# Performance work log

Hardware: AMD Instinct MI355X
Metric: run time of the kernel (lower is better)

Reference implementation:

```python
import jax, jax.numpy as jnp
import numpy as np
import math

B, L, D = 4, 2048, 1024        # batch, x_len, x_dim
QKV, H = 64, 16                # qkv_dim, head_dim (number of heads)


def setup_inputs() -> dict:
    key = jax.random.key(0)
    ks = jax.random.split(key, 10)
    s = 1.0 / math.sqrt(D)
    return {
        "x": jax.random.normal(ks[0], (B, L, D), jnp.float32),
        "encoder_x": jax.random.normal(ks[1], (B, L, D), jnp.float32),
        "Wq": jax.random.normal(ks[2], (D, QKV * H), jnp.float32) * s,
        "bq": jax.random.normal(ks[3], (QKV * H,), jnp.float32) * 0.01,
        "Wk": jax.random.normal(ks[4], (D, QKV * H), jnp.float32) * s,
        "bk": jax.random.normal(ks[5], (QKV * H,), jnp.float32) * 0.01,
        "Wv": jax.random.normal(ks[6], (D, QKV * H), jnp.float32) * s,
        "bv": jax.random.normal(ks[7], (QKV * H,), jnp.float32) * 0.01,
        "Wo": jax.random.normal(ks[8], (QKV * H, D), jnp.float32) * s,
        "bo": jax.random.normal(ks[9], (D,), jnp.float32) * 0.01,
    }


def reference(x, encoder_x, Wq, bq, Wk, bk, Wv, bv, Wo, bo):
    # q,k from encoder_x; v from x  -> [B, L, H, QKV]
    q = (encoder_x @ Wq + bq).reshape(B, L, H, QKV)
    k = (encoder_x @ Wk + bk).reshape(B, L, H, QKV)
    v = (x @ Wv + bv).reshape(B, L, H, QKV)
    # explicit [B,H,L,L] score matrix + softmax over k (faithful to source)
    scores = jax.nn.softmax(
        jnp.einsum("bqhd,bkhd->bhqk", q, k) / math.sqrt(QKV), axis=-1
    )
    # faithful to source einsum 'bvhd,bhqk->bvhd': no shared contraction
    # index, so scores are summed over (q,k) and broadcast onto v per (b,h).
    attn = jnp.einsum("bvhd,bhqk->bvhd", v, scores).reshape(B, L, H * QKV)
    return attn @ Wo + bo
```

## Files before the change

### kernel.cpp

```cpp
#include <hip/hip_runtime.h>
#include <stdint.h>


typedef __attribute__((ext_vector_type(8))) short bf16x8;
typedef __attribute__((ext_vector_type(4))) float f32x4;

typedef __attribute__((address_space(1))) void as1_void;
typedef __attribute__((address_space(3))) void as3_void;
#define GLD16(g, s)                                                          \
  __builtin_amdgcn_global_load_lds((as1_void*)(g), (as3_void*)(s), 16, 0, 0)

__device__ __forceinline__ short f2bf(float f) {
  union { float f; uint32_t u; } v; v.f = f;
  uint32_t r = v.u + 0x7FFFu + ((v.u >> 16) & 1u);
  return (short)(r >> 16);
}

__device__ __forceinline__ bf16x8 pack8(f32x4 a, f32x4 b) {
  union { f32x4 f; uint32_t u[4]; } x, y;
  x.f = a; y.f = b;
#pragma unroll
  for (int t = 0; t < 4; ++t) x.u[t] += 0x8000u;
#pragma unroll
  for (int t = 0; t < 4; ++t) y.u[t] += 0x8000u;
  union { bf16x8 v; uint32_t u[4]; } o;
  o.u[0] = __builtin_amdgcn_perm(x.u[1], x.u[0], 0x07060302);
  o.u[1] = __builtin_amdgcn_perm(x.u[3], x.u[2], 0x07060302);
  o.u[2] = __builtin_amdgcn_perm(y.u[1], y.u[0], 0x07060302);
  o.u[3] = __builtin_amdgcn_perm(y.u[3], y.u[2], 0x07060302);
  return o.v;
}

__global__ __launch_bounds__(256) void wgemm(
    const float* __restrict__ Wo, const float* __restrict__ Wv,
    const float* __restrict__ bv, const float* __restrict__ bo,
    short* __restrict__ Wt, float* __restrict__ biasc) {
  constexpr int BK = 64, NW = 1024;
  __shared__ __align__(16) float Bsf[64 * BK];
  __shared__ __align__(16) float Ts[64 * 36];
  const int b = blockIdx.x, tid = threadIdx.x;

  if (b >= 512) {
    float* red = Bsf;
    const int b3 = b - 512;
    const int nx = tid & 15, ky = tid >> 4;
    const int n = b3 * 16 + nx;
    float s = 0.f;
    for (int k = ky; k < 1024; k += 16)
      s += bv[k] * Wo[(size_t)k * NW + n];
    red[tid] = s;
    __syncthreads();
#pragma unroll
    for (int st = 128; st >= 16; st >>= 1) {
      if (tid < st) red[tid] += red[tid + st];
      __syncthreads();
    }
    if (ky == 0) biasc[n] = 2048.0f * red[nx] + bo[n];
    return;
  }

  const int lane = tid & 63, wave = tid >> 6;
  const int bm = (b >> 4) * 32, bn = (b & 15) * 64;
  const int wm = (wave & 1) * 16, wn = (wave >> 1) * 32;
  const int l15 = lane & 15, quad = lane >> 4;

  f32x4 acc[2];
  acc[0] = (f32x4){0.f, 0.f, 0.f, 0.f};
  acc[1] = (f32x4){0.f, 0.f, 0.f, 0.f};

  const int br = tid >> 4, bc4 = (tid & 15) ^ (br & 7);
  const float* pb = Wv + (size_t)(bn + br) * NW + bc4 * 4;
  float* lb = Bsf + tid * 4;

  const int ajr = tid >> 3, ac4 = (tid & 7) * 4;
  const float* pa = Wo + (size_t)ajr * NW + bm + ac4;

  for (int kt = 0; kt < 1024; kt += BK) {
    float4 va = *(const float4*)(pa);
    float4 vb = *(const float4*)(pa + 32 * (size_t)NW);
    pa += (size_t)BK * NW;
#pragma unroll
    for (int s = 0; s < 4; ++s) GLD16(pb + (size_t)(16 * s) * NW, lb + 1024 * s);
    pb += BK;
    *(float4*)(Ts + ajr * 36 + ac4) = va;
    *(float4*)(Ts + (ajr + 32) * 36 + ac4) = vb;
    __syncthreads();
#pragma unroll
    for (int kk = 0; kk < 2; ++kk) {
      const float* tsp = Ts + ((kk * 4 + quad) * 8) * 36 + wm + l15;
      float av[8];
#pragma unroll
      for (int e = 0; e < 8; ++e) av[e] = tsp[e * 36];
      bf16x8 af = pack8((f32x4){av[0], av[1], av[2], av[3]},
                        (f32x4){av[4], av[5], av[6], av[7]});
#pragma unroll
      for (int j = 0; j < 2; ++j) {
        const int rn = wn + j * 16 + l15;
        const int c4 = kk * 8 + quad * 2;
        f32x4 u0 = *(const f32x4*)(Bsf + (rn * 16 + (c4 ^ (rn & 7))) * 4);
        f32x4 u1 = *(const f32x4*)(Bsf + (rn * 16 + ((c4 + 1) ^ (rn & 7))) * 4);
        acc[j] = __builtin_amdgcn_mfma_f32_16x16x32_bf16(af, pack8(u0, u1),
                                                         acc[j], 0, 0, 0);
      }
    }
    __syncthreads();
  }
#pragma unroll
  for (int j = 0; j < 2; ++j) {
    const int col = bn + wn + j * 16 + l15;
    const int row0 = bm + wm + quad * 4;
#pragma unroll
    for (int r = 0; r < 4; ++r)
      Wt[(size_t)(row0 + r) * NW + col] = f2bf(2048.f * acc[j][r]);
  }
}

__global__ __launch_bounds__(256) void gemm_main(
    const float* __restrict__ X, const short* __restrict__ Bt,
    const float* __restrict__ bias, float* __restrict__ Out,
    int M, int N, int K) {
  constexpr int BK = 64;
  __shared__ __align__(16) char smem[32768];
  short* As = (short*)smem;
  short* Bs = (short*)(smem + 16384);
  const int tid = threadIdx.x, lane = tid & 63, wave = tid >> 6;
  const int b = blockIdx.x;
  const int bm = (b & 63) * 128;
  const int bn = (b >> 6) * 128;
  const int wm = (wave & 1) * 64, wn = (wave >> 1) * 64;
  const int l15 = lane & 15, quad = lane >> 4;

  f32x4 acc[4][4];
#pragma unroll
  for (int i = 0; i < 4; ++i)
#pragma unroll
    for (int j = 0; j < 4; ++j) acc[i][j] = (f32x4){0.f, 0.f, 0.f, 0.f};

  const int srow = tid >> 3, sc8 = (tid & 7) ^ (srow & 7);
  const float* pa = X + (size_t)(bm + srow) * K + sc8 * 8;
  const short* pb = Bt + (size_t)(bn + srow) * K + sc8 * 8;
  short* la = As + tid * 8;
  short* lb = Bs + tid * 8;

  for (int kt = 0; kt < K; kt += BK) {
    float4 a0[4], a1[4];
#pragma unroll
    for (int s = 0; s < 4; ++s) {
      const float* p = pa + (size_t)(32 * s) * K;
      a0[s] = *(const float4*)(p);
      a1[s] = *(const float4*)(p + 4);
    }
#pragma unroll
    for (int s = 0; s < 4; ++s) GLD16(pb + (size_t)(32 * s) * K, lb + 2048 * s);
    pa += BK; pb += BK;
#pragma unroll
    for (int s = 0; s < 4; ++s) {
      *(bf16x8*)(la + 2048 * s) =
          pack8((f32x4){a0[s].x, a0[s].y, a0[s].z, a0[s].w},
                (f32x4){a1[s].x, a1[s].y, a1[s].z, a1[s].w});
    }
    __syncthreads();
#pragma unroll
    for (int kk = 0; kk < 2; ++kk) {
      bf16x8 af[4], bfr[4];
#pragma unroll
      for (int i = 0; i < 4; ++i) {
        const int r = wm + i * 16 + l15;
        af[i] = *(const bf16x8*)(As + r * BK + ((kk * 4 + quad) ^ (r & 7)) * 8);
      }
#pragma unroll
      for (int j = 0; j < 4; ++j) {
        const int r = wn + j * 16 + l15;
        bfr[j] = *(const bf16x8*)(Bs + r * BK + ((kk * 4 + quad) ^ (r & 7)) * 8);
      }
#pragma unroll
      for (int i = 0; i < 4; ++i)
#pragma unroll
        for (int j = 0; j < 4; ++j)
          acc[i][j] = __builtin_amdgcn_mfma_f32_16x16x32_bf16(
              af[i], bfr[j], acc[i][j], 0, 0, 0);
    }
    __syncthreads();
  }

  float* T = (float*)smem + wave * 1088;
#pragma unroll
  for (int i = 0; i < 4; ++i) {
#pragma unroll
    for (int j = 0; j < 4; ++j) {
      const float bb = bias[bn + wn + j * 16 + l15];
#pragma unroll
      for (int r = 0; r < 4; ++r)
        T[(quad * 4 + r) * 68 + j * 16 + l15] = acc[i][j][r] + bb;
    }
#pragma unroll
    for (int p = 0; p < 4; ++p) {
      const int row = (lane >> 4) + 4 * p;
      const int ch = lane & 15;
      f32x4 v = *(const f32x4*)(T + row * 68 + ch * 4);
      *(f32x4*)(Out + (size_t)(bm + wm + i * 16 + row) * N + bn + wn +
                ch * 4) = v;
    }
  }
}

extern "C" void kernel_launch(void* const* d_in, const int* in_sizes, int n_in,
                              void* d_out, int out_size, void* d_ws,
                              size_t ws_size, hipStream_t stream) {
  const float* x  = (const float*)d_in[0];
  const float* Wv = (const float*)d_in[6];
  const float* bv = (const float*)d_in[7];
  const float* Wo = (const float*)d_in[8];
  const float* bo = (const float*)d_in[9];
  float* out = (float*)d_out;

  constexpr int D = 1024, NO = 1024;
  constexpr int M = 8192;

  char* ws = (char*)d_ws;
  short* wt_bf = (short*)(ws);
  float* biasc = (float*)(ws + (2u << 20));

  wgemm<<<576, 256, 0, stream>>>(Wo, Wv, bv, bo, wt_bf, biasc);
  gemm_main<<<(M / 128) * (NO / 128), 256, 0, stream>>>(
      x, wt_bf, biasc, out, M, NO, D);
}
```

Before: 165.3 us.

## Double-buffer A in LDS, load B fragments to registers, halve N tile

Restructures the main GEMM so A tiles are double-buffered in LDS with software prefetch of the next K slice while the current one computes. B fragments are now read directly from global into registers instead of staged through LDS, and the block tile shrinks from 128x128 to 128x64 to double the grid and raise occupancy (launch bounds 4). The aim is to hide global load latency and increase parallelism. The cost is that A is re-read twice as often and B register loads are uncoalesced per lane.

```diff
diff --git a/kernel.cpp b/kernel.cpp
--- a/kernel.cpp
+++ b/kernel.cpp
@@ -115,91 +115,120 @@
   }
 }
 
-__global__ __launch_bounds__(256) void gemm_main(
+__global__ __launch_bounds__(256, 4) void gemm_main(
     const float* __restrict__ X, const short* __restrict__ Bt,
     const float* __restrict__ bias, float* __restrict__ Out,
     int M, int N, int K) {
   constexpr int BK = 64;
   __shared__ __align__(16) char smem[32768];
-  short* As = (short*)smem;
-  short* Bs = (short*)(smem + 16384);
+  short* As0 = (short*)smem;
+  short* As1 = (short*)(smem + 16384);
   const int tid = threadIdx.x, lane = tid & 63, wave = tid >> 6;
   const int b = blockIdx.x;
   const int bm = (b & 63) * 128;
-  const int bn = (b >> 6) * 128;
-  const int wm = (wave & 1) * 64, wn = (wave >> 1) * 64;
+  const int bn = (b >> 6) * 64;
+  const int wm = (wave & 1) * 64, wn = (wave >> 1) * 32;
   const int l15 = lane & 15, quad = lane >> 4;
 
-  f32x4 acc[4][4];
+  f32x4 acc[4][2];
 #pragma unroll
   for (int i = 0; i < 4; ++i)
 #pragma unroll
-    for (int j = 0; j < 4; ++j) acc[i][j] = (f32x4){0.f, 0.f, 0.f, 0.f};
+    for (int j = 0; j < 2; ++j) acc[i][j] = (f32x4){0.f, 0.f, 0.f, 0.f};
 
   const int srow = tid >> 3, sc8 = (tid & 7) ^ (srow & 7);
   const float* pa = X + (size_t)(bm + srow) * K + sc8 * 8;
-  const short* pb = Bt + (size_t)(bn + srow) * K + sc8 * 8;
-  short* la = As + tid * 8;
-  short* lb = Bs + tid * 8;
-
-  for (int kt = 0; kt < K; kt += BK) {
-    float4 a0[4], a1[4];
-#pragma unroll
-    for (int s = 0; s < 4; ++s) {
-      const float* p = pa + (size_t)(32 * s) * K;
-      a0[s] = *(const float4*)(p);
-      a1[s] = *(const float4*)(p + 4);
-    }
-#pragma unroll
-    for (int s = 0; s < 4; ++s) GLD16(pb + (size_t)(32 * s) * K, lb + 2048 * s);
-    pa += BK; pb += BK;
-#pragma unroll
-    for (int s = 0; s < 4; ++s) {
-      *(bf16x8*)(la + 2048 * s) =
-          pack8((f32x4){a0[s].x, a0[s].y, a0[s].z, a0[s].w},
-                (f32x4){a1[s].x, a1[s].y, a1[s].z, a1[s].w});
-    }
-    __syncthreads();
-#pragma unroll
-    for (int kk = 0; kk < 2; ++kk) {
-      bf16x8 af[4], bfr[4];
-#pragma unroll
-      for (int i = 0; i < 4; ++i) {
-        const int r = wm + i * 16 + l15;
-        af[i] = *(const bf16x8*)(As + r * BK + ((kk * 4 + quad) ^ (r & 7)) * 8);
-      }
-#pragma unroll
-      for (int j = 0; j < 4; ++j) {
-        const int r = wn + j * 16 + l15;
-        bfr[j] = *(const bf16x8*)(Bs + r * BK + ((kk * 4 + quad) ^ (r & 7)) * 8);
-      }
-#pragma unroll
-      for (int i = 0; i < 4; ++i)
-#pragma unroll
-        for (int j = 0; j < 4; ++j)
-          acc[i][j] = __builtin_amdgcn_mfma_f32_16x16x32_bf16(
-              af[i], bfr[j], acc[i][j], 0, 0, 0);
-    }
-    __syncthreads();
-  }
-
-  float* T = (float*)smem + wave * 1088;
+  short* la0 = As0 + tid * 8;
+  short* la1 = As1 + tid * 8;
+
+  const short* pb0 = Bt + (size_t)(bn + wn + l15) * K + quad * 8;
+  const short* pb1 = pb0 + 16 * (size_t)K;
+
+  float4 a0[4], a1[4];
+  bf16x8 Bc[4], Bn[4];
+
+#define LOADA(kt)                                                            \
+  {                                                                          \
+    _Pragma("unroll") for (int s = 0; s < 4; ++s) {                          \
+      const float* p = pa + (size_t)(32 * s) * K + (kt);                     \
+      a0[s] = *(const float4*)(p);                                           \
+      a1[s] = *(const float4*)(p + 4);                                       \
+    }                                                                        \
+  }
+#define LOADB(Br, kt)                                                        \
+  {                                                                          \
+    Br[0] = *(const bf16x8*)(pb0 + (kt));                                    \
+    Br[1] = *(const bf16x8*)(pb1 + (kt));                                    \
+    Br[2] = *(const bf16x8*)(pb0 + (kt) + 32);                               \
+    Br[3] = *(const bf16x8*)(pb1 + (kt) + 32);                               \
+  }
+#define PACKWRITE(la)                                                        \
+  {                                                                          \
+    _Pragma("unroll") for (int s = 0; s < 4; ++s)                            \
+        *(bf16x8*)((la) + 2048 * s) =                                        \
+            pack8((f32x4){a0[s].x, a0[s].y, a0[s].z, a0[s].w},               \
+                  (f32x4){a1[s].x, a1[s].y, a1[s].z, a1[s].w});              \
+  }
+#define COMPUTE(As, Br)                                                      \
+  {                                                                          \
+    _Pragma("unroll") for (int kk = 0; kk < 2; ++kk) {                       \
+      bf16x8 af[4];                                                          \
+      _Pragma("unroll") for (int i = 0; i < 4; ++i) {                        \
+        const int r = wm + i * 16 + l15;                                     \
+        af[i] =                                                              \
+            *(const bf16x8*)((As) + r * BK + ((kk * 4 + quad) ^ (r & 7)) * 8);\
+      }                                                                      \
+      _Pragma("unroll") for (int i = 0; i < 4; ++i)                          \
+          _Pragma("unroll") for (int j = 0; j < 2; ++j)                      \
+              acc[i][j] = __builtin_amdgcn_mfma_f32_16x16x32_bf16(           \
+                  af[i], Br[kk * 2 + j], acc[i][j], 0, 0, 0);                \
+    }                                                                        \
+  }
+
+  LOADA(0);
+  LOADB(Bc, 0);
+  PACKWRITE(la0);
+  __syncthreads();
+
+  for (int trip = 0; trip < 8; ++trip) {
+    const int kt_o = trip * 128 + 64;
+    LOADA(kt_o);
+    LOADB(Bn, kt_o);
+    COMPUTE(As0, Bc);
+    PACKWRITE(la1);
+    __syncthreads();
+    if (trip < 7) {
+      const int kt_n = trip * 128 + 128;
+      LOADA(kt_n);
+      LOADB(Bc, kt_n);
+      COMPUTE(As1, Bn);
+      PACKWRITE(la0);
+    } else {
+      COMPUTE(As1, Bn);
+    }
+    __syncthreads();
+  }
+#undef LOADA
+#undef LOADB
+#undef PACKWRITE
+#undef COMPUTE
+
+  float* T = (float*)smem + wave * 576;
 #pragma unroll
   for (int i = 0; i < 4; ++i) {
 #pragma unroll
-    for (int j = 0; j < 4; ++j) {
+    for (int j = 0; j < 2; ++j) {
       const float bb = bias[bn + wn + j * 16 + l15];
 #pragma unroll
       for (int r = 0; r < 4; ++r)
-        T[(quad * 4 + r) * 68 + j * 16 + l15] = acc[i][j][r] + bb;
-    }
-#pragma unroll
-    for (int p = 0; p < 4; ++p) {
-      const int row = (lane >> 4) + 4 * p;
-      const int ch = lane & 15;
-      f32x4 v = *(const f32x4*)(T + row * 68 + ch * 4);
+        T[(quad * 4 + r) * 36 + j * 16 + l15] = acc[i][j][r] + bb;
+    }
+#pragma unroll
+    for (int c = 0; c < 2; ++c) {
+      const int row = (lane >> 3) + 8 * c;
+      f32x4 v = *(const f32x4*)(T + row * 36 + (lane & 7) * 4);
       *(f32x4*)(Out + (size_t)(bm + wm + i * 16 + row) * N + bn + wn +
-                ch * 4) = v;
+                (lane & 7) * 4) = v;
     }
   }
 }
@@ -222,6 +251,6 @@
   float* biasc = (float*)(ws + (2u << 20));
 
   wgemm<<<576, 256, 0, stream>>>(Wo, Wv, bv, bo, wt_bf, biasc);
-  gemm_main<<<(M / 128) * (NO / 128), 256, 0, stream>>>(
+  gemm_main<<<(M / 128) * (NO / 64), 256, 0, stream>>>(
       x, wt_bf, biasc, out, M, NO, D);
 }
```

After: 184.8 us. +11.8%, slower.

## Drop LDS staging in main GEMM; load MFMA fragments directly from global

Applied to the files above, without the earlier changes.

The main GEMM no longer stages A and B tiles through shared memory with barriers. Each of 8 waves (512 threads) now loads its bf16 fragments straight from global memory, converting X from fp32 on the fly, and computes a 64x32 sub-tile. This removes LDS traffic and the per-iteration syncs and raises wave count per block. In exchange it loses the tile reuse across waves, so each X row is fetched by several waves through cache, and the global loads are strided by row rather than coalesced.

```diff
diff --git a/kernel.cpp b/kernel.cpp
--- a/kernel.cpp
+++ b/kernel.cpp
@@ -115,91 +115,84 @@
   }
 }
 
-__global__ __launch_bounds__(256) void gemm_main(
+__global__ __launch_bounds__(512) void gemm_main(
     const float* __restrict__ X, const short* __restrict__ Bt,
     const float* __restrict__ bias, float* __restrict__ Out,
     int M, int N, int K) {
-  constexpr int BK = 64;
-  __shared__ __align__(16) char smem[32768];
-  short* As = (short*)smem;
-  short* Bs = (short*)(smem + 16384);
+  __shared__ __align__(16) float T[8 * 576];
   const int tid = threadIdx.x, lane = tid & 63, wave = tid >> 6;
   const int b = blockIdx.x;
   const int bm = (b & 63) * 128;
   const int bn = (b >> 6) * 128;
-  const int wm = (wave & 1) * 64, wn = (wave >> 1) * 64;
+  const int wm = (wave & 1) * 64, wn = (wave >> 1) * 32;
   const int l15 = lane & 15, quad = lane >> 4;
 
-  f32x4 acc[4][4];
+  f32x4 acc[4][2];
 #pragma unroll
   for (int i = 0; i < 4; ++i)
 #pragma unroll
-    for (int j = 0; j < 4; ++j) acc[i][j] = (f32x4){0.f, 0.f, 0.f, 0.f};
-
-  const int srow = tid >> 3, sc8 = (tid & 7) ^ (srow & 7);
-  const float* pa = X + (size_t)(bm + srow) * K + sc8 * 8;
-  const short* pb = Bt + (size_t)(bn + srow) * K + sc8 * 8;
-  short* la = As + tid * 8;
-  short* lb = Bs + tid * 8;
-
-  for (int kt = 0; kt < K; kt += BK) {
-    float4 a0[4], a1[4];
-#pragma unroll
-    for (int s = 0; s < 4; ++s) {
-      const float* p = pa + (size_t)(32 * s) * K;
-      a0[s] = *(const float4*)(p);
-      a1[s] = *(const float4*)(p + 4);
-    }
-#pragma unroll
-    for (int s = 0; s < 4; ++s) GLD16(pb + (size_t)(32 * s) * K, lb + 2048 * s);
-    pa += BK; pb += BK;
-#pragma unroll
-    for (int s = 0; s < 4; ++s) {
-      *(bf16x8*)(la + 2048 * s) =
-          pack8((f32x4){a0[s].x, a0[s].y, a0[s].z, a0[s].w},
-                (f32x4){a1[s].x, a1[s].y, a1[s].z, a1[s].w});
-    }
-    __syncthreads();
-#pragma unroll
-    for (int kk = 0; kk < 2; ++kk) {
-      bf16x8 af[4], bfr[4];
-#pragma unroll
-      for (int i = 0; i < 4; ++i) {
-        const int r = wm + i * 16 + l15;
-        af[i] = *(const bf16x8*)(As + r * BK + ((kk * 4 + quad) ^ (r & 7)) * 8);
-      }
-#pragma unroll
-      for (int j = 0; j < 4; ++j) {
-        const int r = wn + j * 16 + l15;
-        bfr[j] = *(const bf16x8*)(Bs + r * BK + ((kk * 4 + quad) ^ (r & 7)) * 8);
-      }
-#pragma unroll
-      for (int i = 0; i < 4; ++i)
-#pragma unroll
-        for (int j = 0; j < 4; ++j)
-          acc[i][j] = __builtin_amdgcn_mfma_f32_16x16x32_bf16(
-              af[i], bfr[j], acc[i][j], 0, 0, 0);
-    }
-    __syncthreads();
-  }
-
-  float* T = (float*)smem + wave * 1088;
+    for (int j = 0; j < 2; ++j) acc[i][j] = (f32x4){0.f, 0.f, 0.f, 0.f};
+
+  const float* pa = X + (size_t)(bm + wm + l15) * K + quad * 8;
+  const short* pb0 = Bt + (size_t)(bn + wn + l15) * K + quad * 8;
+  const short* pb1 = pb0 + 16 * (size_t)K;
+
+#pragma unroll 4
+  for (int kt = 0; kt < 1024; kt += 32) {
+    bf16x8 af0, af1, af2, af3, bf0, bf1;
+    {
+      const float* p = pa + kt;
+      float4 u0 = *(const float4*)(p), u1 = *(const float4*)(p + 4);
+      af0 = pack8((f32x4){u0.x, u0.y, u0.z, u0.w},
+                  (f32x4){u1.x, u1.y, u1.z, u1.w});
+    }
+    {
+      const float* p = pa + 16 * (size_t)K + kt;
+      float4 u0 = *(const float4*)(p), u1 = *(const float4*)(p + 4);
+      af1 = pack8((f32x4){u0.x, u0.y, u0.z, u0.w},
+                  (f32x4){u1.x, u1.y, u1.z, u1.w});
+    }
+    {
+      const float* p = pa + 32 * (size_t)K + kt;
+      float4 u0 = *(const float4*)(p), u1 = *(const float4*)(p + 4);
+      af2 = pack8((f32x4){u0.x, u0.y, u0.z, u0.w},
+                  (f32x4){u1.x, u1.y, u1.z, u1.w});
+    }
+    {
+      const float* p = pa + 48 * (size_t)K + kt;
+      float4 u0 = *(const float4*)(p), u1 = *(const float4*)(p + 4);
+      af3 = pack8((f32x4){u0.x, u0.y, u0.z, u0.w},
+                  (f32x4){u1.x, u1.y, u1.z, u1.w});
+    }
+    bf0 = *(const bf16x8*)(pb0 + kt);
+    bf1 = *(const bf16x8*)(pb1 + kt);
+
+    acc[0][0] = __builtin_amdgcn_mfma_f32_16x16x32_bf16(af0, bf0, acc[0][0], 0, 0, 0);
+    acc[0][1] = __builtin_amdgcn_mfma_f32_16x16x32_bf16(af0, bf1, acc[0][1], 0, 0, 0);
+    acc[1][0] = __builtin_amdgcn_mfma_f32_16x16x32_bf16(af1, bf0, acc[1][0], 0, 0, 0);
+    acc[1][1] = __builtin_amdgcn_mfma_f32_16x16x32_bf16(af1, bf1, acc[1][1], 0, 0, 0);
+    acc[2][0] = __builtin_amdgcn_mfma_f32_16x16x32_bf16(af2, bf0, acc[2][0], 0, 0, 0);
+    acc[2][1] = __builtin_amdgcn_mfma_f32_16x16x32_bf16(af2, bf1, acc[2][1], 0, 0, 0);
+    acc[3][0] = __builtin_amdgcn_mfma_f32_16x16x32_bf16(af3, bf0, acc[3][0], 0, 0, 0);
+    acc[3][1] = __builtin_amdgcn_mfma_f32_16x16x32_bf16(af3, bf1, acc[3][1], 0, 0, 0);
+  }
+
+  float* Tw = T + wave * 576;
 #pragma unroll
   for (int i = 0; i < 4; ++i) {
 #pragma unroll
-    for (int j = 0; j < 4; ++j) {
+    for (int j = 0; j < 2; ++j) {
       const float bb = bias[bn + wn + j * 16 + l15];
 #pragma unroll
       for (int r = 0; r < 4; ++r)
-        T[(quad * 4 + r) * 68 + j * 16 + l15] = acc[i][j][r] + bb;
-    }
-#pragma unroll
-    for (int p = 0; p < 4; ++p) {
-      const int row = (lane >> 4) + 4 * p;
-      const int ch = lane & 15;
-      f32x4 v = *(const f32x4*)(T + row * 68 + ch * 4);
+        Tw[(quad * 4 + r) * 36 + j * 16 + l15] = acc[i][j][r] + bb;
+    }
+#pragma unroll
+    for (int c = 0; c < 2; ++c) {
+      const int row = (lane >> 3) + 8 * c;
+      f32x4 v = *(const f32x4*)(Tw + row * 36 + (lane & 7) * 4);
       *(f32x4*)(Out + (size_t)(bm + wm + i * 16 + row) * N + bn + wn +
-                ch * 4) = v;
+                (lane & 7) * 4) = v;
     }
   }
 }
@@ -222,6 +215,6 @@
   float* biasc = (float*)(ws + (2u << 20));
 
   wgemm<<<576, 256, 0, stream>>>(Wo, Wv, bv, bo, wt_bf, biasc);
-  gemm_main<<<(M / 128) * (NO / 128), 256, 0, stream>>>(
+  gemm_main<<<(M / 128) * (NO / 128), 512, 0, stream>>>(
       x, wt_bf, biasc, out, M, NO, D);
 }
```

Measured after the change: 283.6 us. +71.6%, slower.

## Pre-convert x to bf16 in prep kernel and stream A tiles via global_load_lds

Applied to the files above, without the earlier changes.

Adds blocks to the weight-prep kernel that convert the whole fp32 input x into a bf16 workspace buffer. The main GEMM then loads both A and B tiles straight into LDS with async global_load_lds, dropping the per-tile fp32 register loads, packing and LDS stores. This removes conversion work and register pressure from the main loop and halves the A bytes it reads from memory. The cost is an extra full pass that reads 32MB of fp32 and writes 16MB of bf16, plus a larger workspace.

```diff
diff --git a/kernel.cpp b/kernel.cpp
--- a/kernel.cpp
+++ b/kernel.cpp
@@ -31,14 +31,24 @@
   return o.v;
 }
 
-__global__ __launch_bounds__(256) void wgemm(
+__global__ __launch_bounds__(256) void mid(
     const float* __restrict__ Wo, const float* __restrict__ Wv,
     const float* __restrict__ bv, const float* __restrict__ bo,
+    const float* __restrict__ x, short* __restrict__ x_bf,
     short* __restrict__ Wt, float* __restrict__ biasc) {
   constexpr int BK = 64, NW = 1024;
   __shared__ __align__(16) float Bsf[64 * BK];
   __shared__ __align__(16) float Ts[64 * 36];
   const int b = blockIdx.x, tid = threadIdx.x;
+
+  if (b >= 576) {
+    const int i = (b - 576) * 256 + tid;
+    const float4* p = (const float4*)x;
+    float4 a = p[2 * (size_t)i], c = p[2 * (size_t)i + 1];
+    *(bf16x8*)(x_bf + 8 * (size_t)i) =
+        pack8((f32x4){a.x, a.y, a.z, a.w}, (f32x4){c.x, c.y, c.z, c.w});
+    return;
+  }
 
   if (b >= 512) {
     float* red = Bsf;
@@ -116,7 +126,7 @@
 }
 
 __global__ __launch_bounds__(256) void gemm_main(
-    const float* __restrict__ X, const short* __restrict__ Bt,
+    const short* __restrict__ A, const short* __restrict__ Bt,
     const float* __restrict__ bias, float* __restrict__ Out,
     int M, int N, int K) {
   constexpr int BK = 64;
@@ -137,28 +147,17 @@
     for (int j = 0; j < 4; ++j) acc[i][j] = (f32x4){0.f, 0.f, 0.f, 0.f};
 
   const int srow = tid >> 3, sc8 = (tid & 7) ^ (srow & 7);
-  const float* pa = X + (size_t)(bm + srow) * K + sc8 * 8;
+  const short* pa = A + (size_t)(bm + srow) * K + sc8 * 8;
   const short* pb = Bt + (size_t)(bn + srow) * K + sc8 * 8;
   short* la = As + tid * 8;
   short* lb = Bs + tid * 8;
 
   for (int kt = 0; kt < K; kt += BK) {
-    float4 a0[4], a1[4];
-#pragma unroll
-    for (int s = 0; s < 4; ++s) {
-      const float* p = pa + (size_t)(32 * s) * K;
-      a0[s] = *(const float4*)(p);
-      a1[s] = *(const float4*)(p + 4);
-    }
+#pragma unroll
+    for (int s = 0; s < 4; ++s) GLD16(pa + (size_t)(32 * s) * K, la + 2048 * s);
 #pragma unroll
     for (int s = 0; s < 4; ++s) GLD16(pb + (size_t)(32 * s) * K, lb + 2048 * s);
     pa += BK; pb += BK;
-#pragma unroll
-    for (int s = 0; s < 4; ++s) {
-      *(bf16x8*)(la + 2048 * s) =
-          pack8((f32x4){a0[s].x, a0[s].y, a0[s].z, a0[s].w},
-                (f32x4){a1[s].x, a1[s].y, a1[s].z, a1[s].w});
-    }
     __syncthreads();
 #pragma unroll
     for (int kk = 0; kk < 2; ++kk) {
@@ -218,10 +217,11 @@
   constexpr int M = 8192;
 
   char* ws = (char*)d_ws;
-  short* wt_bf = (short*)(ws);
-  float* biasc = (float*)(ws + (2u << 20));
-
-  wgemm<<<576, 256, 0, stream>>>(Wo, Wv, bv, bo, wt_bf, biasc);
+  short* x_bf  = (short*)(ws);
+  short* wt_bf = (short*)(ws + (16u << 20));
+  float* biasc = (float*)(ws + (18u << 20));
+
+  mid<<<4672, 256, 0, stream>>>(Wo, Wv, bv, bo, x, x_bf, wt_bf, biasc);
   gemm_main<<<(M / 128) * (NO / 128), 256, 0, stream>>>(
-      x, wt_bf, biasc, out, M, NO, D);
-}
+      x_bf, wt_bf, biasc, out, M, NO, D);
+}
```

After: 156.7 us. -5.2%, faster.
